# Optimization experiments

Hardware: AMD Instinct MI355X
Metric: run time of the kernel (lower is better)

## Reference

```python
import jax, jax.numpy as jnp
import numpy as np


def setup_inputs() -> dict:
    key = jax.random.key(0)
    ks = jax.random.split(key, 7)
    IN, OUT, B = 8192, 8192, 256
    return {
        "x": jax.random.normal(ks[0], (B, IN), dtype=jnp.float32),
        "mu_weights": jax.random.normal(ks[1], (OUT, IN), dtype=jnp.float32) * 0.02,
        "rho_weights": jax.random.normal(ks[2], (OUT, IN), dtype=jnp.float32) * 0.1 - 3.0,
        "mu_bias": jax.random.normal(ks[3], (OUT,), dtype=jnp.float32) * 0.02,
        "rho_bias": jax.random.normal(ks[4], (OUT,), dtype=jnp.float32) * 0.1 - 3.0,
        "eps_w": jax.random.normal(ks[5], (OUT, IN), dtype=jnp.float32),
        "eps_b": jax.random.normal(ks[6], (OUT,), dtype=jnp.float32),
    }


def reference(x, mu_weights, rho_weights, mu_bias, rho_bias, eps_w, eps_b):
    # sigma = log(1 + exp(rho))  (softplus); W = mu + sigma * eps
    sigma_w = jnp.log1p(jnp.exp(rho_weights))
    W = mu_weights + sigma_w * eps_w            # [out, in]
    out = jnp.einsum("bi,oi->bo", x, W)          # x @ W.T -> [b, out]
    sigma_b = jnp.log1p(jnp.exp(rho_bias))
    b = mu_bias + sigma_b * eps_b                # [out]
    return out + b
```

## Files before the change

### kernel.cpp

```cpp
#include <hip/hip_runtime.h>

typedef _Float16 f16;
typedef _Float16 f16x8 __attribute__((ext_vector_type(8)));
typedef float f32x4 __attribute__((ext_vector_type(4)));

#define IN_DIM  8192
#define OUT_DIM 8192
#define BATCH   256
#define BK      32
#define BN      128
#define NSPLIT  4
#define KSPL    (IN_DIM / NSPLIT)
#define NSTEP   (KSPL / BK)

__device__ __forceinline__ float softplus_f(float r) {
    return __logf(1.0f + __expf(r));
}

#define ISSUE_W(S, Ma,Mb,Ra,Rb,Ea,Eb) do {                                   \
    const int o_ = (S) * BK;                                                 \
    Ma = *(const f32x4*)(mup + o_);   Mb = *(const f32x4*)(mup + o_ + 4);    \
    Ra = *(const f32x4*)(rhp + o_);   Rb = *(const f32x4*)(rhp + o_ + 4);    \
    Ea = *(const f32x4*)(epp + o_);   Eb = *(const f32x4*)(epp + o_ + 4);    \
} while (0)

#define COMMIT_W(BUF, Ma,Mb,Ra,Rb,Ea,Eb) do {                                \
    f16x8 wv_;                                                               \
    _Pragma("unroll")                                                        \
    for (int q_ = 0; q_ < 4; ++q_) {                                         \
        wv_[q_]   = (f16)(Ma[q_] + softplus_f(Ra[q_]) * Ea[q_]);             \
        wv_[4+q_] = (f16)(Mb[q_] + softplus_f(Rb[q_]) * Eb[q_]);             \
    }                                                                        \
    *(f16x8*)&sm[BUF][b_st] = wv_;                                           \
} while (0)

#define ISSUE_A(S) do {                                                      \
    const int o_ = (S) * BK;                                                 \
    Ap0 = *(const f32x4*)(xa0 + o_);  Ap1 = *(const f32x4*)(xa0 + o_ + 4);   \
    Ap2 = *(const f32x4*)(xa1 + o_);  Ap3 = *(const f32x4*)(xa1 + o_ + 4);   \
    Ap4 = *(const f32x4*)(xa2 + o_);  Ap5 = *(const f32x4*)(xa2 + o_ + 4);   \
    Ap6 = *(const f32x4*)(xa3 + o_);  Ap7 = *(const f32x4*)(xa3 + o_ + 4);   \
} while (0)

#define CVT_A() do {                                                         \
    _Pragma("unroll")                                                        \
    for (int q_ = 0; q_ < 4; ++q_) {                                         \
        af0[q_] = (f16)Ap0[q_];  af0[4+q_] = (f16)Ap1[q_];                   \
        af1[q_] = (f16)Ap2[q_];  af1[4+q_] = (f16)Ap3[q_];                   \
        af2[q_] = (f16)Ap4[q_];  af2[4+q_] = (f16)Ap5[q_];                   \
        af3[q_] = (f16)Ap6[q_];  af3[4+q_] = (f16)Ap7[q_];                   \
    }                                                                        \
} while (0)

#define MSTEP(BUF) do {                                                      \
    f16x8 bf_[4];                                                            \
    _Pragma("unroll")                                                        \
    for (int j_ = 0; j_ < 4; ++j_) {                                         \
        const int br_ = wn * 64 + j_ * 16 + (lane & 15);                     \
        bf_[j_] = *(const f16x8*)&sm[BUF][br_ * BK +                         \
                    (((lane >> 4) ^ ((br_ >> 1) & 3)) << 3)];                \
    }                                                                        \
    _Pragma("unroll")                                                        \
    for (int j_ = 0; j_ < 4; ++j_) {                                         \
        acc[0][j_] = __builtin_amdgcn_mfma_f32_16x16x32_f16(af0, bf_[j_], acc[0][j_], 0, 0, 0); \
        acc[1][j_] = __builtin_amdgcn_mfma_f32_16x16x32_f16(af1, bf_[j_], acc[1][j_], 0, 0, 0); \
        acc[2][j_] = __builtin_amdgcn_mfma_f32_16x16x32_f16(af2, bf_[j_], acc[2][j_], 0, 0, 0); \
        acc[3][j_] = __builtin_amdgcn_mfma_f32_16x16x32_f16(af3, bf_[j_], acc[3][j_], 0, 0, 0); \
    }                                                                        \
} while (0)

#define BARRIER() do {                                                       \
    asm volatile("s_waitcnt lgkmcnt(0)" ::: "memory");                       \
    __builtin_amdgcn_s_barrier();                                            \
} while (0)

__global__ __launch_bounds__(512, 2)
void vl_main(const float* __restrict__ x,
             const float* __restrict__ muw,
             const float* __restrict__ rhow,
             const float* __restrict__ epsw,
             const float* __restrict__ mub,
             const float* __restrict__ rhob,
             const float* __restrict__ epsb,
             float* __restrict__ out)
{
    __shared__ __align__(16) f16 sm[2][BN * BK];

    const int t    = threadIdx.x;
    const int lane = t & 63;
    const int wid  = t >> 6;
    const int wm   = wid >> 1;
    const int wn   = wid & 1;

    const int bx = blockIdx.x;
    const int x7 = bx & 7;
    const int sk = x7 >> 1;
    const int nb = (x7 & 1) * 32 + (bx >> 3);
    const int k_base = sk * KSPL;
    const int n_base = nb * BN;

    const int slot = t & 3;
    const int row  = t >> 2;
    const size_t woff = (size_t)(n_base + row) * IN_DIM + k_base + slot * 8;
    const float* mup = muw  + woff;
    const float* rhp = rhow + woff;
    const float* epp = epsw + woff;

    const int b_st = row * BK + ((slot ^ ((row >> 1) & 3)) << 3);

    const int kf = (lane >> 4) * 8;
    const float* xa0 = x + (size_t)(wm * 64 +  0 + (lane & 15)) * IN_DIM + k_base + kf;
    const float* xa1 = x + (size_t)(wm * 64 + 16 + (lane & 15)) * IN_DIM + k_base + kf;
    const float* xa2 = x + (size_t)(wm * 64 + 32 + (lane & 15)) * IN_DIM + k_base + kf;
    const float* xa3 = x + (size_t)(wm * 64 + 48 + (lane & 15)) * IN_DIM + k_base + kf;

    f32x4 acc[4][4];
#pragma unroll
    for (int i = 0; i < 4; ++i)
#pragma unroll
        for (int j = 0; j < 4; ++j)
            acc[i][j] = (f32x4){0.f, 0.f, 0.f, 0.f};

    f32x4 Ap0, Ap1, Ap2, Ap3, Ap4, Ap5, Ap6, Ap7;
    f32x4 M0a, M0b, R0a, R0b, E0a, E0b;
    f32x4 M1a, M1b, R1a, R1b, E1a, E1b;
    f16x8 af0, af1, af2, af3;

    ISSUE_A(0);
    ISSUE_W(0, M0a, M0b, R0a, R0b, E0a, E0b);
    ISSUE_W(1, M1a, M1b, R1a, R1b, E1a, E1b);
    COMMIT_W(0, M0a, M0b, R0a, R0b, E0a, E0b);
    BARRIER();

    for (int s = 0; s < NSTEP; s += 2) {
        CVT_A();
        ISSUE_A(s + 1);
        if (s + 2 < NSTEP) ISSUE_W(s + 2, M0a, M0b, R0a, R0b, E0a, E0b);
        MSTEP(0);
        COMMIT_W(1, M1a, M1b, R1a, R1b, E1a, E1b);
        BARRIER();
        CVT_A();
        if (s + 2 < NSTEP) ISSUE_A(s + 2);
        if (s + 3 < NSTEP) ISSUE_W(s + 3, M1a, M1b, R1a, R1b, E1a, E1b);
        MSTEP(1);
        if (s + 2 < NSTEP) {
            COMMIT_W(0, M0a, M0b, R0a, R0b, E0a, E0b);
            BARRIER();
        }
    }

    float bias[4] = {0.f, 0.f, 0.f, 0.f};
    if (sk == 0) {
#pragma unroll
        for (int j = 0; j < 4; ++j) {
            const int c = n_base + wn * 64 + j * 16 + (lane & 15);
            bias[j] = mub[c] + softplus_f(rhob[c]) * epsb[c];
        }
    }
#pragma unroll
    for (int i = 0; i < 4; ++i) {
        const int r = wm * 64 + i * 16 + ((lane >> 4) << 2);
#pragma unroll
        for (int j = 0; j < 4; ++j) {
            const int c = n_base + wn * 64 + j * 16 + (lane & 15);
            float* po = out + (size_t)r * OUT_DIM + c;
#pragma unroll
            for (int q = 0; q < 4; ++q)
                atomicAdd(po + (size_t)q * OUT_DIM, acc[i][j][q] + bias[j]);
        }
    }
}

extern "C" void kernel_launch(void* const* d_in, const int* in_sizes, int n_in,
                              void* d_out, int out_size, void* d_ws, size_t ws_size,
                              hipStream_t stream) {
    (void)in_sizes; (void)n_in; (void)d_ws; (void)ws_size;
    const float* x    = (const float*)d_in[0];
    const float* muw  = (const float*)d_in[1];
    const float* rhow = (const float*)d_in[2];
    const float* mub  = (const float*)d_in[3];
    const float* rhob = (const float*)d_in[4];
    const float* epsw = (const float*)d_in[5];
    const float* epsb = (const float*)d_in[6];
    float* out = (float*)d_out;

    hipMemsetAsync(out, 0, (size_t)out_size * sizeof(float), stream);
    vl_main<<<dim3(256), dim3(512), 0, stream>>>(x, muw, rhow, epsw,
                                                 mub, rhob, epsb, out);
}
```

Baseline: 259.5 us.

## Specialize warps into loader roles, stage x in LDS, pre-convert x to fp16

Blocks grow to 1024 threads. The first half of the threads load and convert x tiles into a new shared-memory A buffer, and the second half loads mu/rho/eps and builds the fp16 W tile. All 16 waves then run MFMAs from LDS with a 4x4 wave grid, so each wave now owns 64x32 outputs. A separate pre-kernel converts x to fp16 into the workspace, which halves the x read traffic at the cost of an extra launch. The risks are lower per-thread load parallelism for W (each W thread does one role), more LDS use, and a non-trivial occupancy target of 4 blocks of 1024.

```diff
diff --git a/kernel.cpp b/kernel.cpp
--- a/kernel.cpp
+++ b/kernel.cpp
@@ -31,41 +31,53 @@
         wv_[q_]   = (f16)(Ma[q_] + softplus_f(Ra[q_]) * Ea[q_]);             \
         wv_[4+q_] = (f16)(Mb[q_] + softplus_f(Rb[q_]) * Eb[q_]);             \
     }                                                                        \
-    *(f16x8*)&sm[BUF][b_st] = wv_;                                           \
+    *(f16x8*)&smW[BUF][wst] = wv_;                                           \
 } while (0)
 
 #define ISSUE_A(S) do {                                                      \
-    const int o_ = (S) * BK;                                                 \
-    Ap0 = *(const f32x4*)(xa0 + o_);  Ap1 = *(const f32x4*)(xa0 + o_ + 4);   \
-    Ap2 = *(const f32x4*)(xa1 + o_);  Ap3 = *(const f32x4*)(xa1 + o_ + 4);   \
-    Ap4 = *(const f32x4*)(xa2 + o_);  Ap5 = *(const f32x4*)(xa2 + o_ + 4);   \
-    Ap6 = *(const f32x4*)(xa3 + o_);  Ap7 = *(const f32x4*)(xa3 + o_ + 4);   \
-} while (0)
-
-#define CVT_A() do {                                                         \
+    if constexpr (XF16) {                                                    \
+        Xa = *(const f16x8*)(xap + (S) * BK);                                \
+        Xb = *(const f16x8*)(xap + (S) * BK + 8);                            \
+    } else {                                                                 \
+        F0 = *(const f32x4*)(xfp + (S) * BK);                                \
+        F1 = *(const f32x4*)(xfp + (S) * BK + 4);                            \
+        F2 = *(const f32x4*)(xfp + (S) * BK + 8);                            \
+        F3 = *(const f32x4*)(xfp + (S) * BK + 12);                           \
+    }                                                                        \
+} while (0)
+
+#define COMMIT_A(BUF) do {                                                   \
+    f16x8 a0_, a1_;                                                          \
+    if constexpr (XF16) {                                                    \
+        a0_ = Xa; a1_ = Xb;                                                  \
+    } else {                                                                 \
+        _Pragma("unroll")                                                    \
+        for (int q_ = 0; q_ < 4; ++q_) {                                     \
+            a0_[q_] = (f16)F0[q_];  a0_[4+q_] = (f16)F1[q_];                 \
+            a1_[q_] = (f16)F2[q_];  a1_[4+q_] = (f16)F3[q_];                 \
+        }                                                                    \
+    }                                                                        \
+    *(f16x8*)&smA[BUF][ast0] = a0_;                                          \
+    *(f16x8*)&smA[BUF][ast1] = a1_;                                          \
+} while (0)
+
+#define MSTEP(B) do {                                                        \
+    const int rr_ = lane & 15;                                               \
+    const int ko_ = lane >> 4;                                               \
+    f16x8 bf_[2];                                                            \
     _Pragma("unroll")                                                        \
-    for (int q_ = 0; q_ < 4; ++q_) {                                         \
-        af0[q_] = (f16)Ap0[q_];  af0[4+q_] = (f16)Ap1[q_];                   \
-        af1[q_] = (f16)Ap2[q_];  af1[4+q_] = (f16)Ap3[q_];                   \
-        af2[q_] = (f16)Ap4[q_];  af2[4+q_] = (f16)Ap5[q_];                   \
-        af3[q_] = (f16)Ap6[q_];  af3[4+q_] = (f16)Ap7[q_];                   \
-    }                                                                        \
-} while (0)
-
-#define MSTEP(BUF) do {                                                      \
-    f16x8 bf_[4];                                                            \
+    for (int j_ = 0; j_ < 2; ++j_) {                                         \
+        const int br_ = wn * 32 + j_ * 16 + rr_;                             \
+        bf_[j_] = *(const f16x8*)&smW[B][br_ * BK + ((ko_ ^ ((br_ >> 1) & 3)) << 3)]; \
+    }                                                                        \
     _Pragma("unroll")                                                        \
-    for (int j_ = 0; j_ < 4; ++j_) {                                         \
-        const int br_ = wn * 64 + j_ * 16 + (lane & 15);                     \
-        bf_[j_] = *(const f16x8*)&sm[BUF][br_ * BK +                         \
-                    (((lane >> 4) ^ ((br_ >> 1) & 3)) << 3)];                \
-    }                                                                        \
-    _Pragma("unroll")                                                        \
-    for (int j_ = 0; j_ < 4; ++j_) {                                         \
-        acc[0][j_] = __builtin_amdgcn_mfma_f32_16x16x32_f16(af0, bf_[j_], acc[0][j_], 0, 0, 0); \
-        acc[1][j_] = __builtin_amdgcn_mfma_f32_16x16x32_f16(af1, bf_[j_], acc[1][j_], 0, 0, 0); \
-        acc[2][j_] = __builtin_amdgcn_mfma_f32_16x16x32_f16(af2, bf_[j_], acc[2][j_], 0, 0, 0); \
-        acc[3][j_] = __builtin_amdgcn_mfma_f32_16x16x32_f16(af3, bf_[j_], acc[3][j_], 0, 0, 0); \
+    for (int i_ = 0; i_ < 4; ++i_) {                                         \
+        const int ar_ = wm * 64 + i_ * 16 + rr_;                             \
+        const f16x8 af_ = *(const f16x8*)&smA[B][ar_ * BK + ((ko_ ^ ((ar_ >> 1) & 3)) << 3)]; \
+        _Pragma("unroll")                                                    \
+        for (int j_ = 0; j_ < 2; ++j_)                                       \
+            acc[i_][j_] = __builtin_amdgcn_mfma_f32_16x16x32_f16(            \
+                af_, bf_[j_], acc[i_][j_], 0, 0, 0);                         \
     }                                                                        \
 } while (0)
 
@@ -74,8 +86,10 @@
     __builtin_amdgcn_s_barrier();                                            \
 } while (0)
 
-__global__ __launch_bounds__(512, 2)
+template <bool XF16>
+__global__ __launch_bounds__(1024, 4)
 void vl_main(const float* __restrict__ x,
+             const f16*   __restrict__ x16,
              const float* __restrict__ muw,
              const float* __restrict__ rhow,
              const float* __restrict__ epsw,
@@ -84,13 +98,14 @@
              const float* __restrict__ epsb,
              float* __restrict__ out)
 {
-    __shared__ __align__(16) f16 sm[2][BN * BK];
+    __shared__ __align__(16) f16 smA[2][BATCH * BK];
+    __shared__ __align__(16) f16 smW[2][BN * BK];
 
     const int t    = threadIdx.x;
     const int lane = t & 63;
     const int wid  = t >> 6;
-    const int wm   = wid >> 1;
-    const int wn   = wid & 1;
+    const int wm   = wid >> 2;
+    const int wn   = wid & 3;
 
     const int bx = blockIdx.x;
     const int x7 = bx & 7;
@@ -99,61 +114,66 @@
     const int k_base = sk * KSPL;
     const int n_base = nb * BN;
 
-    const int slot = t & 3;
-    const int row  = t >> 2;
-    const size_t woff = (size_t)(n_base + row) * IN_DIM + k_base + slot * 8;
+    const bool isA = (t < 512);
+
+    const int arow = (t & 511) >> 1;
+    const int ahalf = t & 1;
+    const f16*   xap = x16 + (size_t)arow * IN_DIM + k_base + ahalf * 16;
+    const float* xfp = x   + (size_t)arow * IN_DIM + k_base + ahalf * 16;
+    const int aswr = (arow >> 1) & 3;
+    const int ast0 = arow * BK + (((ahalf * 2 + 0) ^ aswr) << 3);
+    const int ast1 = arow * BK + (((ahalf * 2 + 1) ^ aswr) << 3);
+
+    const int u = t & 511;
+    const int wrow = u >> 2;
+    const int wslot = u & 3;
+    const size_t woff = (size_t)(n_base + wrow) * IN_DIM + k_base + wslot * 8;
     const float* mup = muw  + woff;
     const float* rhp = rhow + woff;
     const float* epp = epsw + woff;
-
-    const int b_st = row * BK + ((slot ^ ((row >> 1) & 3)) << 3);
-
-    const int kf = (lane >> 4) * 8;
-    const float* xa0 = x + (size_t)(wm * 64 +  0 + (lane & 15)) * IN_DIM + k_base + kf;
-    const float* xa1 = x + (size_t)(wm * 64 + 16 + (lane & 15)) * IN_DIM + k_base + kf;
-    const float* xa2 = x + (size_t)(wm * 64 + 32 + (lane & 15)) * IN_DIM + k_base + kf;
-    const float* xa3 = x + (size_t)(wm * 64 + 48 + (lane & 15)) * IN_DIM + k_base + kf;
-
-    f32x4 acc[4][4];
+    const int wst = wrow * BK + ((wslot ^ ((wrow >> 1) & 3)) << 3);
+
+    f32x4 acc[4][2];
 #pragma unroll
     for (int i = 0; i < 4; ++i)
 #pragma unroll
-        for (int j = 0; j < 4; ++j)
+        for (int j = 0; j < 2; ++j)
             acc[i][j] = (f32x4){0.f, 0.f, 0.f, 0.f};
 
-    f32x4 Ap0, Ap1, Ap2, Ap3, Ap4, Ap5, Ap6, Ap7;
-    f32x4 M0a, M0b, R0a, R0b, E0a, E0b;
-    f32x4 M1a, M1b, R1a, R1b, E1a, E1b;
-    f16x8 af0, af1, af2, af3;
-
-    ISSUE_A(0);
-    ISSUE_W(0, M0a, M0b, R0a, R0b, E0a, E0b);
-    ISSUE_W(1, M1a, M1b, R1a, R1b, E1a, E1b);
-    COMMIT_W(0, M0a, M0b, R0a, R0b, E0a, E0b);
+    f16x8 Xa, Xb;
+    f32x4 F0, F1, F2, F3;
+    f32x4 M0a,M0b,R0a,R0b,E0a,E0b;
+    f32x4 M1a,M1b,R1a,R1b,E1a,E1b;
+
+    if (isA) { ISSUE_A(0); }
+    else {
+        ISSUE_W(0, M0a,M0b,R0a,R0b,E0a,E0b);
+        ISSUE_W(1, M1a,M1b,R1a,R1b,E1a,E1b);
+    }
+    if (isA) { COMMIT_A(0); ISSUE_A(1); }
+    else     { COMMIT_W(0, M0a,M0b,R0a,R0b,E0a,E0b); }
     BARRIER();
 
     for (int s = 0; s < NSTEP; s += 2) {
-        CVT_A();
-        ISSUE_A(s + 1);
-        if (s + 2 < NSTEP) ISSUE_W(s + 2, M0a, M0b, R0a, R0b, E0a, E0b);
+        if (!isA && s + 2 < NSTEP) ISSUE_W(s + 2, M0a,M0b,R0a,R0b,E0a,E0b);
         MSTEP(0);
-        COMMIT_W(1, M1a, M1b, R1a, R1b, E1a, E1b);
+        if (isA) { COMMIT_A(1); if (s + 2 < NSTEP) ISSUE_A(s + 2); }
+        else     { COMMIT_W(1, M1a,M1b,R1a,R1b,E1a,E1b); }
         BARRIER();
-        CVT_A();
-        if (s + 2 < NSTEP) ISSUE_A(s + 2);
-        if (s + 3 < NSTEP) ISSUE_W(s + 3, M1a, M1b, R1a, R1b, E1a, E1b);
+        if (!isA && s + 3 < NSTEP) ISSUE_W(s + 3, M1a,M1b,R1a,R1b,E1a,E1b);
         MSTEP(1);
         if (s + 2 < NSTEP) {
-            COMMIT_W(0, M0a, M0b, R0a, R0b, E0a, E0b);
-            BARRIER();
+            if (isA) { COMMIT_A(0); ISSUE_A(s + 3 < NSTEP ? s + 3 : NSTEP - 1); }
+            else     { COMMIT_W(0, M0a,M0b,R0a,R0b,E0a,E0b); }
         }
-    }
-
-    float bias[4] = {0.f, 0.f, 0.f, 0.f};
+        BARRIER();
+    }
+
+    float bias[2] = {0.f, 0.f};
     if (sk == 0) {
 #pragma unroll
-        for (int j = 0; j < 4; ++j) {
-            const int c = n_base + wn * 64 + j * 16 + (lane & 15);
+        for (int j = 0; j < 2; ++j) {
+            const int c = n_base + wn * 32 + j * 16 + (lane & 15);
             bias[j] = mub[c] + softplus_f(rhob[c]) * epsb[c];
         }
     }
@@ -161,8 +181,8 @@
     for (int i = 0; i < 4; ++i) {
         const int r = wm * 64 + i * 16 + ((lane >> 4) << 2);
 #pragma unroll
-        for (int j = 0; j < 4; ++j) {
-            const int c = n_base + wn * 64 + j * 16 + (lane & 15);
+        for (int j = 0; j < 2; ++j) {
+            const int c = n_base + wn * 32 + j * 16 + (lane & 15);
             float* po = out + (size_t)r * OUT_DIM + c;
 #pragma unroll
             for (int q = 0; q < 4; ++q)
@@ -171,10 +191,19 @@
     }
 }
 
+__global__ void cvt_x16(const float* __restrict__ x, f16* __restrict__ x16) {
+    const int i = (blockIdx.x * 256 + threadIdx.x) * 4;
+    const f32x4 v = *(const f32x4*)(x + i);
+    f16 o[4];
+#pragma unroll
+    for (int q = 0; q < 4; ++q) o[q] = (f16)v[q];
+    *(unsigned long long*)(x16 + i) = *(unsigned long long*)o;
+}
+
 extern "C" void kernel_launch(void* const* d_in, const int* in_sizes, int n_in,
                               void* d_out, int out_size, void* d_ws, size_t ws_size,
                               hipStream_t stream) {
-    (void)in_sizes; (void)n_in; (void)d_ws; (void)ws_size;
+    (void)in_sizes; (void)n_in;
     const float* x    = (const float*)d_in[0];
     const float* muw  = (const float*)d_in[1];
     const float* rhow = (const float*)d_in[2];
@@ -185,6 +214,15 @@
     float* out = (float*)d_out;
 
     hipMemsetAsync(out, 0, (size_t)out_size * sizeof(float), stream);
-    vl_main<<<dim3(256), dim3(512), 0, stream>>>(x, muw, rhow, epsw,
-                                                 mub, rhob, epsb, out);
-}
+
+    const size_t xelems = (size_t)BATCH * IN_DIM;
+    if (ws_size >= xelems * sizeof(f16)) {
+        f16* x16 = (f16*)d_ws;
+        cvt_x16<<<dim3(xelems / 1024), dim3(256), 0, stream>>>(x, x16);
+        vl_main<true><<<dim3(256), dim3(1024), 0, stream>>>(
+            x, x16, muw, rhow, epsw, mub, rhob, epsb, out);
+    } else {
+        vl_main<false><<<dim3(256), dim3(1024), 0, stream>>>(
+            x, nullptr, muw, rhow, epsw, mub, rhob, epsb, out);
+    }
+}
```

New measurement: 235.6 us. 1.1x faster.
